# Kernel optimization log

Measured on AMD Instinct MI355X. Metric: run time of the kernel, lower is better.

## Reference

```python
import jax, jax.numpy as jnp
import numpy as np

ACT_MIN, ACT_MAX = -127.0, 127.0      # 8-bit symmetric
W_MIN, W_MAX = -127.0, 127.0          # 8-bit symmetric
B_MIN, B_MAX = -32767.0, 32767.0      # 16-bit symmetric
ALPHA = 10.0                          # clipped-ReLU ceiling


def fake_quant(x, min_v, max_v):
    # 'scale' quantization: per-tensor symmetric scale from max-abs,
    # round -> clamp -> dequant; straight-through estimator for grads.
    scale = max_v / jnp.max(jnp.abs(x))
    q = jnp.clip(jnp.round(x * scale), min_v, max_v) / scale
    return x + jax.lax.stop_gradient(q - x)


def qconv(x, w, b, stride, pad):
    wq = fake_quant(w, W_MIN, W_MAX)
    bq = fake_quant(b, B_MIN, B_MAX)
    y = jax.lax.conv_general_dilated(
        x, wq, (stride, stride), [(pad, pad), (pad, pad)],
        dimension_numbers=('NCHW', 'OIHW', 'NCHW'))
    return y + bq[None, :, None, None]


def qrelu(x):
    return fake_quant(jnp.clip(x, 0.0, ALPHA), ACT_MIN, ACT_MAX)


def maxpool(x, k, s, p):
    return jax.lax.reduce_window(
        x, -jnp.inf, jax.lax.max,
        (1, 1, k, k), (1, 1, s, s),
        [(0, 0), (0, 0), (p, p), (p, p)])


def setup_inputs() -> dict:
    key = jax.random.key(0)
    ks = jax.random.split(key, 13)

    def kaiming(k, shape):
        fan_in = int(np.prod(shape[1:]))
        return jax.random.normal(k, shape, jnp.float32) * np.sqrt(2.0 / fan_in)

    return {
        'x':  jax.random.normal(ks[0], (4096, 1, 32, 32), jnp.float32),
        'w1': kaiming(ks[1], (32, 1, 3, 3)),  'b1': jnp.zeros((32,), jnp.float32) + 0.01,
        'w2': kaiming(ks[2], (64, 32, 3, 3)), 'b2': jnp.zeros((64,), jnp.float32) + 0.01,
        'w3': kaiming(ks[3], (16, 64, 1, 1)), 'b3': jnp.zeros((16,), jnp.float32) + 0.01,
        'w4': kaiming(ks[4], (16, 16, 3, 3)), 'b4': jnp.zeros((16,), jnp.float32) + 0.01,
        'w5': kaiming(ks[5], (64, 16, 1, 1)), 'b5': jnp.zeros((64,), jnp.float32) + 0.01,
        'wl': kaiming(ks[6], (10, 64)),       'bl': jnp.zeros((10,), jnp.float32) + 0.01,
    }


def reference(x, w1, b1, w2, b2, w3, b3, w4, b4, w5, b5, wl, bl):
    x = fake_quant(x, ACT_MIN, ACT_MAX)           # quantize input acts
    x_skip1 = maxpool(x, 5, 4, 2)                 # [B,1,8,8]
    out = qrelu(qconv(x, w1, b1, 2, 1))           # [B,32,16,16]
    out = qconv(out, w2, b2, 2, 1)                # [B,64,8,8]
    out = qrelu(out + x_skip1)                    # broadcast 1ch skip over 64ch
    x_skip2 = maxpool(out, 3, 2, 1)               # [B,64,4,4]
    out = qrelu(qconv(out, w3, b3, 1, 0))         # [B,16,8,8]
    out = qrelu(qconv(out, w4, b4, 2, 1))         # [B,16,4,4]
    out = qconv(out, w5, b5, 1, 0)                # [B,64,4,4]
    out = qrelu(out + x_skip2)
    out = jnp.mean(out, axis=(2, 3))              # avgpool 4x4 -> [B,64]
    wq = fake_quant(wl, W_MIN, W_MAX)
    bq = fake_quant(bl, B_MIN, B_MAX)
    return out @ wq.T + bq                        # [B,10]
```

## Files before the change

kernel.cpp:

```cpp
#include <hip/hip_runtime.h>

#define BATCH 4096

typedef __attribute__((ext_vector_type(8))) short bf16x8;
typedef __attribute__((ext_vector_type(4))) float f32x4;

constexpr int OFF_MAXARR = 1024;
constexpr int OFF_W1Q = 8192;
constexpr int OFF_W2Q = OFF_W1Q + 288;
constexpr int OFF_W3Q = OFF_W2Q + 18432;
constexpr int OFF_W4Q = OFF_W3Q + 1024;
constexpr int OFF_W5Q = OFF_W4Q + 2304;
constexpr int OFF_WLQ = OFF_W5Q + 1024;
constexpr int OFF_B1Q = OFF_WLQ + 640;
constexpr int OFF_B2Q = OFF_B1Q + 32;
constexpr int OFF_B3Q = OFF_B2Q + 64;
constexpr int OFF_B4Q = OFF_B3Q + 16;
constexpr int OFF_B5Q = OFF_B4Q + 16;
constexpr int OFF_BLQ = OFF_B5Q + 64;
constexpr int OFF_W1I = 32768;
constexpr int OFF_W2I = OFF_W1I + 512;
constexpr int OFF_W3I = OFF_W2I + 9216;
constexpr size_t OFF_SK1F = 49152;
constexpr size_t OFF_V2   = OFF_SK1F + (size_t)BATCH * 64;
constexpr size_t OFF_SK2I = OFF_V2 + (size_t)BATCH * 4096;
constexpr size_t OFF_A3   = OFF_SK2I + (size_t)BATCH * 512;
constexpr size_t OFF_A4   = OFF_A3 + (size_t)BATCH * 1024;
constexpr size_t OFF_A5   = OFF_A4 + (size_t)BATCH * 256;
constexpr size_t WS_FLOATS_NEEDED = OFF_A5 + (size_t)BATCH * 1024;

#define A1_S   40
#define A1_ROW (18 * A1_S)

__device__ __forceinline__ float fq(float x, float scale, float maxv) {
    float q = rintf(x * scale);
    q = fminf(fmaxf(q, -maxv), maxv);
    return q / scale;
}

__device__ __forceinline__ short int_to_bf16_bits(float v) {
    return (short)(__float_as_uint(v) >> 16);
}

__device__ __forceinline__ float bf16_bits_to_float(short b) {
    return __uint_as_float(((unsigned)(unsigned short)b) << 16);
}

__device__ __forceinline__ void block_max_spread(float v, unsigned* arr, float* red4) {
#pragma unroll
    for (int off = 32; off; off >>= 1) v = fmaxf(v, __shfl_xor(v, off, 64));
    int tid = threadIdx.x;
    if ((tid & 63) == 0) red4[tid >> 6] = v;
    __syncthreads();
    if (tid == 0) {
        float m = fmaxf(fmaxf(red4[0], red4[1]), fmaxf(red4[2], red4[3]));
        atomicMax(&arr[(blockIdx.x & 63) << 4], __float_as_uint(m));
    }
    __syncthreads();
}

__device__ __forceinline__ float load_spread_max(const unsigned* arr, float* bc) {
    int tid = threadIdx.x;
    if (tid < 64) {
        float v = __uint_as_float(arr[tid << 4]);
#pragma unroll
        for (int off = 32; off; off >>= 1) v = fmaxf(v, __shfl_xor(v, off, 64));
        if (tid == 0) *bc = v;
    }
    __syncthreads();
    return *bc;
}

__device__ __forceinline__ void stage_xq(const float* xi, float sx, short* xt_q, int tid) {
    for (int i = tid; i < 1024; i += 256) {
        int ih = i >> 5, iw = i & 31;
        float q = rintf(xi[i] * sx);
        q = fminf(fmaxf(q, -127.f), 127.f);
        xt_q[(ih + 1) * 34 + (iw + 1)] = int_to_bf16_bits(q);
    }
}

__device__ __forceinline__ void build_qx1(const short* xt_q, short* qx1, int tid) {
    int oh = tid >> 4, ow = tid & 15;
    short* dst = qx1 + tid * 32;
#pragma unroll
    for (int kh = 0; kh < 3; kh++)
#pragma unroll
        for (int kw = 0; kw < 3; kw++)
            dst[kh * 3 + kw] = xt_q[(oh * 2 + kh) * 34 + (ow * 2 + kw)];
}

__device__ __forceinline__ void conv1_mfma(const short* qx1, const bf16x8 w1b[2],
                                           int lane, int wv, f32x4 acc[4][2]) {
#pragma unroll
    for (int mb = 0; mb < 4; mb++) {
        bf16x8 a = *(const bf16x8*)(qx1 + ((wv * 4 + mb) * 16 + (lane & 15)) * 32
                                    + (lane >> 4) * 8);
#pragma unroll
        for (int nb = 0; nb < 2; nb++)
            acc[mb][nb] = __builtin_amdgcn_mfma_f32_16x16x32_bf16(a, w1b[nb], acc[mb][nb], 0, 0, 0);
    }
}

struct WeightArgs {
    const float* src[12];
    float*       dst[12];
    int          n[12];
    float        maxv[12];
};

__global__ __launch_bounds__(256) void k_weights(WeightArgs a) {
    int t = blockIdx.x;
    const float* s = a.src[t];
    float* d = a.dst[t];
    int n = a.n[t];
    float maxv = a.maxv[t];
    __shared__ float red[256];
    int tid = threadIdx.x;
    float m = 0.f;
    for (int i = tid; i < n; i += 256) m = fmaxf(m, fabsf(s[i]));
    red[tid] = m;
    __syncthreads();
    for (int sft = 128; sft > 0; sft >>= 1) {
        if (tid < sft) red[tid] = fmaxf(red[tid], red[tid + sft]);
        __syncthreads();
    }
    float scale = maxv / red[0];
    for (int i = tid; i < n; i += 256) {
        float q = rintf(s[i] * scale);
        q = fminf(fmaxf(q, -maxv), maxv);
        d[i] = q / scale;
    }
}

__global__ __launch_bounds__(256) void k_prep_w1(const float* __restrict__ w1,
                                                 short* __restrict__ w1i,
                                                 float* __restrict__ inv_sw_slot) {
    __shared__ float red[256];
    int tid = threadIdx.x;
    float m = 0.f;
    for (int i = tid; i < 288; i += 256) m = fmaxf(m, fabsf(w1[i]));
    red[tid] = m;
    __syncthreads();
    for (int s = 128; s > 0; s >>= 1) {
        if (tid < s) red[tid] = fmaxf(red[tid], red[tid + s]);
        __syncthreads();
    }
    float maxw = red[0];
    float sw = 127.f / maxw;
    if (tid == 0) *inv_sw_slot = maxw / 127.f;
    for (int i = tid; i < 1024; i += 256) w1i[i] = 0;
    __syncthreads();
    for (int i = tid; i < 288; i += 256) {
        int oc = i / 9, t = i % 9;
        float q = rintf(w1[i] * sw);
        q = fminf(fmaxf(q, -127.f), 127.f);
        w1i[oc * 32 + t] = int_to_bf16_bits(q);
    }
}

__global__ __launch_bounds__(256) void k_prep_w2(const float* __restrict__ w2,
                                                 short* __restrict__ w2i,
                                                 float* __restrict__ inv_sw_slot) {
    __shared__ float red[256];
    int tid = threadIdx.x;
    float m = 0.f;
    for (int i = tid; i < 18432; i += 256) m = fmaxf(m, fabsf(w2[i]));
    red[tid] = m;
    __syncthreads();
    for (int s = 128; s > 0; s >>= 1) {
        if (tid < s) red[tid] = fmaxf(red[tid], red[tid + s]);
        __syncthreads();
    }
    float maxw = red[0];
    float sw = 127.f / maxw;
    if (tid == 0) *inv_sw_slot = maxw / 127.f;
    for (int i = tid; i < 18432; i += 256) {
        int oc = i / 288, r = i % 288, ic = r / 9, t = r % 9;
        float q = rintf(w2[i] * sw);
        q = fminf(fmaxf(q, -127.f), 127.f);
        w2i[oc * 288 + t * 32 + ic] = int_to_bf16_bits(q);
    }
}

__global__ __launch_bounds__(256) void k_prep_w3(const float* __restrict__ w3,
                                                 short* __restrict__ w3i,
                                                 float* __restrict__ inv_sw_slot) {
    __shared__ float red[256];
    int tid = threadIdx.x;
    float m = 0.f;
    for (int i = tid; i < 1024; i += 256) m = fmaxf(m, fabsf(w3[i]));
    red[tid] = m;
    __syncthreads();
    for (int s = 128; s > 0; s >>= 1) {
        if (tid < s) red[tid] = fmaxf(red[tid], red[tid + s]);
        __syncthreads();
    }
    float maxw = red[0];
    float sw = 127.f / maxw;
    if (tid == 0) *inv_sw_slot = maxw / 127.f;
    for (int i = tid; i < 1024; i += 256) {
        float q = rintf(w3[i] * sw);
        q = fminf(fmaxf(q, -127.f), 127.f);
        w3i[i] = int_to_bf16_bits(q);
    }
}

__global__ __launch_bounds__(256) void k_absmax(const float4* __restrict__ x, int n4,
                                                unsigned* arr) {
    __shared__ float red4[4];
    float m = 0.f;
    for (int i = blockIdx.x * 256 + threadIdx.x; i < n4; i += gridDim.x * 256) {
        float4 v = x[i];
        m = fmaxf(m, fmaxf(fmaxf(fabsf(v.x), fabsf(v.y)), fmaxf(fabsf(v.z), fabsf(v.w))));
    }
    block_max_spread(m, arr, red4);
}

__global__ __launch_bounds__(256) void k_s1(const float* __restrict__ x,
                                            const short* __restrict__ w1i,
                                            const float* __restrict__ b1q,
                                            const unsigned* xmaxarr,
                                            const float* __restrict__ inv_sw1p,
                                            float* __restrict__ skip1f,
                                            unsigned* m1arr) {
    __shared__ short xt_q[34 * 34];
    __shared__ short qx1[256 * 32];
    __shared__ float red4[4];
    __shared__ float bc0;
    int tid = threadIdx.x, lane = tid & 63, wv = tid >> 6;
    float xmax = load_spread_max(xmaxarr, &bc0);
    float sx = 127.f / xmax;
    float inv1 = (*inv_sw1p) / sx;
    bf16x8 w1b[2];
#pragma unroll
    for (int nb = 0; nb < 2; nb++)
        w1b[nb] = *(const bf16x8*)(w1i + (nb * 16 + (lane & 15)) * 32 + (lane >> 4) * 8);
    float bias1[2] = {b1q[lane & 15], b1q[16 + (lane & 15)]};

    for (int i = tid; i < 34 * 34; i += 256) xt_q[i] = 0;
    for (int i = tid; i < 256 * 16; i += 256) ((int*)qx1)[i] = 0;

    float lmax = 0.f;
    for (int li = 0; li < 4; li++) {
        int img = blockIdx.x * 4 + li;
        __syncthreads();
        stage_xq(x + (size_t)img * 1024, sx, xt_q, tid);
        __syncthreads();
        build_qx1(xt_q, qx1, tid);
        if (tid < 64) {
            int soh = tid >> 3, sow = tid & 7;
            float m = -INFINITY;
            int h0 = soh * 4 - 2, w0 = sow * 4 - 2;
            for (int kh = 0; kh < 5; kh++) {
                int ih = h0 + kh;
                if (ih < 0 || ih >= 32) continue;
                for (int kw = 0; kw < 5; kw++) {
                    int iw = w0 + kw;
                    if (iw < 0 || iw >= 32) continue;
                    m = fmaxf(m, bf16_bits_to_float(xt_q[(ih + 1) * 34 + (iw + 1)]));
                }
            }
            skip1f[img * 64 + tid] = m / sx;
        }
        __syncthreads();
        f32x4 acc[4][2] = {};
        conv1_mfma(qx1, w1b, lane, wv, acc);
#pragma unroll
        for (int mb = 0; mb < 4; mb++)
#pragma unroll
            for (int nb = 0; nb < 2; nb++)
#pragma unroll
                for (int r = 0; r < 4; r++) {
                    float v = acc[mb][nb][r] * inv1 + bias1[nb];
                    lmax = fmaxf(lmax, fminf(fmaxf(v, 0.f), 10.f));
                }
    }
    block_max_spread(lmax, m1arr, red4);
}

__global__ __launch_bounds__(256) void k_s2(const float* __restrict__ x,
                                            const short* __restrict__ w1i,
                                            const float* __restrict__ b1q,
                                            const short* __restrict__ w2i,
                                            const float* __restrict__ b2q,
                                            const float* __restrict__ skip1f,
                                            const unsigned* xmaxarr, const unsigned* m1arr,
                                            const float* __restrict__ inv_sw1p,
                                            const float* __restrict__ inv_sw2p,
                                            float* __restrict__ v2w,
                                            unsigned* m2arr) {
    __shared__ short xt_q[34 * 34];
    __shared__ short qx1[256 * 32];
    __shared__ short a1t[18 * A1_ROW];
    __shared__ float sk1s[64];
    __shared__ float red4[4];
    __shared__ float bc0, bc1;
    int tid = threadIdx.x, lane = tid & 63, wv = tid >> 6;
    float xmax = load_spread_max(xmaxarr, &bc0);
    float m1 = load_spread_max(m1arr, &bc1);
    float sx = 127.f / xmax;
    float inv1 = (*inv_sw1p) / sx;
    float s1q = 127.f / m1;
    float inv2 = (m1 / 127.f) * (*inv_sw2p);

    bf16x8 w1b[2];
#pragma unroll
    for (int nb = 0; nb < 2; nb++)
        w1b[nb] = *(const bf16x8*)(w1i + (nb * 16 + (lane & 15)) * 32 + (lane >> 4) * 8);
    float bias1[2] = {b1q[lane & 15], b1q[16 + (lane & 15)]};
    int oc2 = wv * 16 + (lane & 15);
    bf16x8 bw2[9];
#pragma unroll
    for (int t = 0; t < 9; t++)
        bw2[t] = *(const bf16x8*)(w2i + oc2 * 288 + t * 32 + (lane >> 4) * 8);
    float bias2 = b2q[oc2];

    for (int i = tid; i < 34 * 34; i += 256) xt_q[i] = 0;
    for (int i = tid; i < 256 * 16; i += 256) ((int*)qx1)[i] = 0;
    for (int i = tid; i < 18 * A1_ROW / 2; i += 256) ((int*)a1t)[i] = 0;

    float lmax = 0.f;
    for (int li = 0; li < 4; li++) {
        int img = blockIdx.x * 4 + li;
        __syncthreads();
        stage_xq(x + (size_t)img * 1024, sx, xt_q, tid);
        if (tid < 64) sk1s[tid] = skip1f[img * 64 + tid];
        __syncthreads();
        build_qx1(xt_q, qx1, tid);
        __syncthreads();
        f32x4 acc1[4][2] = {};
        conv1_mfma(qx1, w1b, lane, wv, acc1);
#pragma unroll
        for (int mb = 0; mb < 4; mb++)
#pragma unroll
            for (int nb = 0; nb < 2; nb++)
#pragma unroll
                for (int r = 0; r < 4; r++) {
                    float v = acc1[mb][nb][r] * inv1 + bias1[nb];
                    v = fminf(fmaxf(v, 0.f), 10.f);
                    float q = fminf(rintf(v * s1q), 127.f);
                    int pos = (wv * 4 + mb) * 16 + (lane >> 4) * 4 + r;
                    int oc = nb * 16 + (lane & 15);
                    a1t[((pos >> 4) + 1) * A1_ROW + ((pos & 15) + 1) * A1_S + oc] =
                        int_to_bf16_bits(q);
                }
        __syncthreads();
        float* vo = v2w + (size_t)img * 4096;
#pragma unroll
        for (int mb = 0; mb < 4; mb++) {
            int m = mb * 16 + (lane & 15);
            int oh = m >> 3, ow = m & 7;
            const short* abase = a1t + (oh * 2) * A1_ROW + (ow * 2) * A1_S + (lane >> 4) * 8;
            f32x4 acc = {0.f, 0.f, 0.f, 0.f};
#pragma unroll
            for (int kh = 0; kh < 3; kh++)
#pragma unroll
                for (int kw = 0; kw < 3; kw++) {
                    bf16x8 av = *(const bf16x8*)(abase + kh * A1_ROW + kw * A1_S);
                    acc = __builtin_amdgcn_mfma_f32_16x16x32_bf16(av, bw2[kh * 3 + kw], acc, 0, 0, 0);
                }
            float4 vv;
            float* vvp = (float*)&vv;
#pragma unroll
            for (int r = 0; r < 4; r++) {
                int pos = mb * 16 + (lane >> 4) * 4 + r;
                float v = acc[r] * inv2 + bias2 + sk1s[pos];
                v = fminf(fmaxf(v, 0.f), 10.f);
                vvp[r] = v;
                lmax = fmaxf(lmax, v);
            }
            *(float4*)(vo + oc2 * 64 + mb * 16 + (lane >> 4) * 4) = vv;
        }
    }
    block_max_spread(lmax, m2arr, red4);
}

__global__ __launch_bounds__(256) void k_s3(const float* __restrict__ v2w,
                                            const short* __restrict__ w3i,
                                            const float* __restrict__ b3q,
                                            const unsigned* m2arr,
                                            const float* __restrict__ inv_sw3p,
                                            float* __restrict__ a3w,
                                            short* __restrict__ sk2q,
                                            unsigned* m3arr) {
    __shared__ short a2q[64 * 64];
    __shared__ float red4[4];
    __shared__ float bc0;
    int tid = threadIdx.x, lane = tid & 63, wv = tid >> 6;
    float m2 = load_spread_max(m2arr, &bc0);
    float s2 = 127.f / m2;
    float inv3 = (m2 / 127.f) * (*inv_sw3p);
    int oc2 = wv * 16 + (lane & 15);
    bf16x8 bw3[2];
#pragma unroll
    for (int t = 0; t < 2; t++)
        bw3[t] = *(const bf16x8*)(w3i + (lane & 15) * 64 + t * 32 + (lane >> 4) * 8);
    float bias3 = b3q[lane & 15];

    float lmax = 0.f;
    for (int li = 0; li < 4; li++) {
        int img = blockIdx.x * 4 + li;
        __syncthreads();
        const float* vi = v2w + (size_t)img * 4096;
#pragma unroll
        for (int mb = 0; mb < 4; mb++) {
            float4 vv = *(const float4*)(vi + oc2 * 64 + mb * 16 + (lane >> 4) * 4);
            const float* vvp = (const float*)&vv;
#pragma unroll
            for (int r = 0; r < 4; r++) {
                int pos = mb * 16 + (lane >> 4) * 4 + r;
                float q = fminf(rintf(vvp[r] * s2), 127.f);
                a2q[pos * 64 + oc2] = int_to_bf16_bits(q);
            }
        }
        __syncthreads();
        const short* abase = a2q + (wv * 16 + (lane & 15)) * 64 + (lane >> 4) * 8;
        f32x4 acc = {0.f, 0.f, 0.f, 0.f};
#pragma unroll
        for (int t = 0; t < 2; t++) {
            bf16x8 av = *(const bf16x8*)(abase + t * 32);
            acc = __builtin_amdgcn_mfma_f32_16x16x32_bf16(av, bw3[t], acc, 0, 0, 0);
        }
        float* a3o = a3w + (size_t)img * 1024;
#pragma unroll
        for (int r = 0; r < 4; r++) {
            int pos = wv * 16 + (lane >> 4) * 4 + r;
            float v = acc[r] * inv3 + bias3;
            v = fminf(fmaxf(v, 0.f), 10.f);
            a3o[(lane & 15) * 64 + pos] = v;
            lmax = fmaxf(lmax, v);
        }
        short* sko = sk2q + (size_t)img * 1024;
#pragma unroll
        for (int r = 0; r < 4; ++r) {
            int idx = tid * 4 + r;
            int c = idx >> 4, pp = idx & 15, soh = pp >> 2, sow = pp & 3;
            float m = -INFINITY;
            for (int kh = 0; kh < 3; kh++) {
                int ih = soh * 2 - 1 + kh;
                if (ih < 0 || ih >= 8) continue;
                for (int kw = 0; kw < 3; kw++) {
                    int iw = sow * 2 - 1 + kw;
                    if (iw < 0 || iw >= 8) continue;
                    m = fmaxf(m, bf16_bits_to_float(a2q[(ih * 8 + iw) * 64 + c]));
                }
            }
            sko[idx] = int_to_bf16_bits(m);
        }
    }
    block_max_spread(lmax, m3arr, red4);
}

__global__ __launch_bounds__(256) void k_conv4(const float* __restrict__ a3,
                                               const float* __restrict__ w4q,
                                               const float* __restrict__ b4q,
                                               const unsigned* m3arr,
                                               float* __restrict__ a4,
                                               unsigned* m4arr) {
    __shared__ float tile[16 * 10 * 10];
    __shared__ float red4[4];
    __shared__ float bc0;
    int b = blockIdx.x, tid = threadIdx.x;
    float m3 = load_spread_max(m3arr, &bc0);
    float s3 = 127.f / m3;
    for (int i = tid; i < 1600; i += 256) tile[i] = 0.f;
    __syncthreads();
    const float* ai = a3 + (size_t)b * 1024;
    for (int i = tid; i < 1024; i += 256) {
        int ic = i >> 6, p = i & 63, ih = p >> 3, iw = p & 7;
        float q = rintf(ai[i] * s3);
        q = fminf(fmaxf(q, -127.f), 127.f);
        tile[ic * 100 + (ih + 1) * 10 + (iw + 1)] = q / s3;
    }
    __syncthreads();
    int oc = tid >> 4, p = tid & 15, oh = p >> 2, ow = p & 3;
    float acc = b4q[oc];
    const float* w = w4q + oc * 144;
    for (int ic = 0; ic < 16; ic++) {
        const float* tin = tile + ic * 100 + (oh * 2) * 10 + (ow * 2);
        const float* wc = w + ic * 9;
#pragma unroll
        for (int kh = 0; kh < 3; kh++)
#pragma unroll
            for (int kw = 0; kw < 3; kw++)
                acc += tin[kh * 10 + kw] * wc[kh * 3 + kw];
    }
    float v = fminf(fmaxf(acc, 0.f), 10.f);
    a4[(size_t)b * 256 + tid] = v;
    block_max_spread(v, m4arr, red4);
}

__global__ __launch_bounds__(256) void k_conv5(const float* __restrict__ a4,
                                               const float* __restrict__ w5q,
                                               const float* __restrict__ b5q,
                                               const short* __restrict__ sk2q,
                                               const unsigned* m2arr,
                                               const unsigned* m4arr,
                                               float* __restrict__ a5,
                                               unsigned* m5arr) {
    __shared__ float tin[256];
    __shared__ float red4[4];
    __shared__ float bc0, bc1;
    int b = blockIdx.x, tid = threadIdx.x;
    float m2 = load_spread_max(m2arr, &bc0);
    float m4 = load_spread_max(m4arr, &bc1);
    float s4 = 127.f / m4;
    float invs2 = m2 / 127.f;
    const float* ai = a4 + (size_t)b * 256;
    {
        float q = rintf(ai[tid] * s4);
        q = fminf(fmaxf(q, -127.f), 127.f);
        tin[tid] = q / s4;
    }
    __syncthreads();
    int p = tid & 15, ocb = tid >> 4;
    float lmax = 0.f;
    float* o = a5 + (size_t)b * 1024;
    for (int j = 0; j < 4; j++) {
        int oc = ocb * 4 + j;
        float acc = b5q[oc];
        const float* w = w5q + oc * 16;
#pragma unroll
        for (int ic = 0; ic < 16; ic++) acc += tin[ic * 16 + p] * w[ic];
        acc += bf16_bits_to_float(sk2q[(size_t)b * 1024 + oc * 16 + p]) * invs2;
        float v = fminf(fmaxf(acc, 0.f), 10.f);
        o[oc * 16 + p] = v;
        lmax = fmaxf(lmax, v);
    }
    block_max_spread(lmax, m5arr, red4);
}

__global__ __launch_bounds__(64) void k_head(const float* __restrict__ a5,
                                             const unsigned* m5arr,
                                             const float* __restrict__ wlq,
                                             const float* __restrict__ blq,
                                             float* __restrict__ out) {
    __shared__ float h[64];
    __shared__ float bc0;
    int b = blockIdx.x, c = threadIdx.x;
    float m5 = load_spread_max(m5arr, &bc0);
    float s5 = 127.f / m5;
    const float* ai = a5 + (size_t)b * 1024 + c * 16;
    float sum = 0.f;
#pragma unroll
    for (int p = 0; p < 16; p++) sum += fq(ai[p], s5, 127.f);
    h[c] = sum * (1.f / 16.f);
    __syncthreads();
    if (c < 10) {
        float acc = blq[c];
        const float* w = wlq + c * 64;
        for (int ic = 0; ic < 64; ic++) acc = fmaf(h[ic], w[ic], acc);
        out[(size_t)b * 10 + c] = acc;
    }
}

extern "C" void kernel_launch(void* const* d_in, const int* in_sizes, int n_in,
                              void* d_out, int out_size, void* d_ws, size_t ws_size,
                              hipStream_t stream) {
    const float* x  = (const float*)d_in[0];
    const float* w1 = (const float*)d_in[1];
    const float* b1 = (const float*)d_in[2];
    const float* w2 = (const float*)d_in[3];
    const float* b2 = (const float*)d_in[4];
    const float* w3 = (const float*)d_in[5];
    const float* b3 = (const float*)d_in[6];
    const float* w4 = (const float*)d_in[7];
    const float* b4 = (const float*)d_in[8];
    const float* w5 = (const float*)d_in[9];
    const float* b5 = (const float*)d_in[10];
    const float* wl = (const float*)d_in[11];
    const float* bl = (const float*)d_in[12];

    if (ws_size < WS_FLOATS_NEEDED * sizeof(float)) return;

    float* ws = (float*)d_ws;
    unsigned* slots = (unsigned*)d_ws;
    unsigned* marr[6];
    for (int k = 0; k < 6; k++) marr[k] = slots + OFF_MAXARR + k * 1024;
    short* w1i = (short*)(ws + OFF_W1I);
    short* w2i = (short*)(ws + OFF_W2I);
    short* w3i = (short*)(ws + OFF_W3I);

    hipMemsetAsync(d_ws, 0, 32768, stream);

    WeightArgs wa;
    const float* srcs[12] = {w1, w2, w3, w4, w5, wl, b1, b2, b3, b4, b5, bl};
    const int    ns[12]   = {288, 18432, 1024, 2304, 1024, 640, 32, 64, 16, 16, 64, 10};
    const int    offs[12] = {OFF_W1Q, OFF_W2Q, OFF_W3Q, OFF_W4Q, OFF_W5Q, OFF_WLQ,
                             OFF_B1Q, OFF_B2Q, OFF_B3Q, OFF_B4Q, OFF_B5Q, OFF_BLQ};
    const float  mv[12]   = {127.f, 127.f, 127.f, 127.f, 127.f, 127.f,
                             32767.f, 32767.f, 32767.f, 32767.f, 32767.f, 32767.f};
    for (int i = 0; i < 12; i++) {
        wa.src[i] = srcs[i];
        wa.dst[i] = ws + offs[i];
        wa.n[i] = ns[i];
        wa.maxv[i] = mv[i];
    }
    k_weights<<<12, 256, 0, stream>>>(wa);
    k_prep_w1<<<1, 256, 0, stream>>>(w1, w1i, ws + 8);
    k_prep_w2<<<1, 256, 0, stream>>>(w2, w2i, ws + 6);
    k_prep_w3<<<1, 256, 0, stream>>>(w3, w3i, ws + 7);

    k_absmax<<<512, 256, 0, stream>>>((const float4*)x, BATCH * 256, marr[0]);
    k_s1<<<BATCH / 4, 256, 0, stream>>>(x, w1i, ws + OFF_B1Q, marr[0], ws + 8,
                                        ws + OFF_SK1F, marr[1]);
    k_s2<<<BATCH / 4, 256, 0, stream>>>(x, w1i, ws + OFF_B1Q, w2i, ws + OFF_B2Q,
                                        ws + OFF_SK1F, marr[0], marr[1], ws + 8, ws + 6,
                                        ws + OFF_V2, marr[2]);
    k_s3<<<BATCH / 4, 256, 0, stream>>>(ws + OFF_V2, w3i, ws + OFF_B3Q, marr[2], ws + 7,
                                        ws + OFF_A3, (short*)(ws + OFF_SK2I), marr[3]);
    k_conv4<<<BATCH, 256, 0, stream>>>(ws + OFF_A3, ws + OFF_W4Q, ws + OFF_B4Q, marr[3],
                                       ws + OFF_A4, marr[4]);
    k_conv5<<<BATCH, 256, 0, stream>>>(ws + OFF_A4, ws + OFF_W5Q, ws + OFF_B5Q,
                                       (const short*)(ws + OFF_SK2I), marr[2], marr[4],
                                       ws + OFF_A5, marr[5]);
    k_head<<<BATCH, 64, 0, stream>>>(ws + OFF_A5, marr[5], ws + OFF_WLQ, ws + OFF_BLQ,
                                     (float*)d_out);
}
```

Before: 255.7 us.

## Merge prep kernels into one launch and build conv1 fragments directly from LDS

Folds the five weight/bias/input absmax prep kernels into a single launch that dispatches work by block index, with 256 blocks (previously 512) for the input absmax. It also drops the qx1 im2col staging buffer in k_s1/k_s2, gathering conv1 MFMA A-fragments straight from the padded input tile. This removes launch overhead, one LDS round trip and a barrier per image, and frees 16KB of LDS per block. The cost is scattered 2-byte LDS reads when forming each fragment and less parallelism in the absmax pass.

```diff
diff --git a/kernel.cpp b/kernel.cpp
--- a/kernel.cpp
+++ b/kernel.cpp
@@ -80,141 +80,118 @@
     }
 }
 
-__device__ __forceinline__ void build_qx1(const short* xt_q, short* qx1, int tid) {
-    int oh = tid >> 4, ow = tid & 15;
-    short* dst = qx1 + tid * 32;
-#pragma unroll
-    for (int kh = 0; kh < 3; kh++)
-#pragma unroll
-        for (int kw = 0; kw < 3; kw++)
-            dst[kh * 3 + kw] = xt_q[(oh * 2 + kh) * 34 + (ow * 2 + kw)];
-}
-
-__device__ __forceinline__ void conv1_mfma(const short* qx1, const bf16x8 w1b[2],
-                                           int lane, int wv, f32x4 acc[4][2]) {
-#pragma unroll
-    for (int mb = 0; mb < 4; mb++) {
-        bf16x8 a = *(const bf16x8*)(qx1 + ((wv * 4 + mb) * 16 + (lane & 15)) * 32
-                                    + (lane >> 4) * 8);
-#pragma unroll
-        for (int nb = 0; nb < 2; nb++)
-            acc[mb][nb] = __builtin_amdgcn_mfma_f32_16x16x32_bf16(a, w1b[nb], acc[mb][nb], 0, 0, 0);
-    }
-}
-
-struct WeightArgs {
+__device__ __forceinline__ bf16x8 load_a1frag(const short* xt_q, int pos, int kslot) {
+    bf16x8 a = {0, 0, 0, 0, 0, 0, 0, 0};
+    int oh = pos >> 4, ow = pos & 15;
+    const short* base = xt_q + (oh * 2) * 34 + ow * 2;
+    if (kslot == 0) {
+        a[0] = base[0];  a[1] = base[1];  a[2] = base[2];
+        a[3] = base[34]; a[4] = base[35]; a[5] = base[36];
+        a[6] = base[68]; a[7] = base[69];
+    } else if (kslot == 1) {
+        a[0] = base[70];
+    }
+    return a;
+}
+
+struct PrepArgs {
     const float* src[12];
     float*       dst[12];
     int          n[12];
     float        maxv[12];
+    const float* w1; short* w1i; float* inv1;
+    const float* w2; short* w2i; float* inv2;
+    const float* w3; short* w3i; float* inv3;
+    const float4* x; int n4; unsigned* xarr;
 };
 
-__global__ __launch_bounds__(256) void k_weights(WeightArgs a) {
-    int t = blockIdx.x;
-    const float* s = a.src[t];
-    float* d = a.dst[t];
-    int n = a.n[t];
-    float maxv = a.maxv[t];
+__global__ __launch_bounds__(256) void k_prep(PrepArgs P) {
     __shared__ float red[256];
-    int tid = threadIdx.x;
-    float m = 0.f;
-    for (int i = tid; i < n; i += 256) m = fmaxf(m, fabsf(s[i]));
-    red[tid] = m;
-    __syncthreads();
-    for (int sft = 128; sft > 0; sft >>= 1) {
-        if (tid < sft) red[tid] = fmaxf(red[tid], red[tid + sft]);
-        __syncthreads();
-    }
-    float scale = maxv / red[0];
-    for (int i = tid; i < n; i += 256) {
-        float q = rintf(s[i] * scale);
-        q = fminf(fmaxf(q, -maxv), maxv);
-        d[i] = q / scale;
-    }
-}
-
-__global__ __launch_bounds__(256) void k_prep_w1(const float* __restrict__ w1,
-                                                 short* __restrict__ w1i,
-                                                 float* __restrict__ inv_sw_slot) {
-    __shared__ float red[256];
-    int tid = threadIdx.x;
-    float m = 0.f;
-    for (int i = tid; i < 288; i += 256) m = fmaxf(m, fabsf(w1[i]));
-    red[tid] = m;
-    __syncthreads();
-    for (int s = 128; s > 0; s >>= 1) {
-        if (tid < s) red[tid] = fmaxf(red[tid], red[tid + s]);
-        __syncthreads();
-    }
-    float maxw = red[0];
-    float sw = 127.f / maxw;
-    if (tid == 0) *inv_sw_slot = maxw / 127.f;
-    for (int i = tid; i < 1024; i += 256) w1i[i] = 0;
-    __syncthreads();
-    for (int i = tid; i < 288; i += 256) {
-        int oc = i / 9, t = i % 9;
-        float q = rintf(w1[i] * sw);
-        q = fminf(fmaxf(q, -127.f), 127.f);
-        w1i[oc * 32 + t] = int_to_bf16_bits(q);
-    }
-}
-
-__global__ __launch_bounds__(256) void k_prep_w2(const float* __restrict__ w2,
-                                                 short* __restrict__ w2i,
-                                                 float* __restrict__ inv_sw_slot) {
-    __shared__ float red[256];
-    int tid = threadIdx.x;
-    float m = 0.f;
-    for (int i = tid; i < 18432; i += 256) m = fmaxf(m, fabsf(w2[i]));
-    red[tid] = m;
-    __syncthreads();
-    for (int s = 128; s > 0; s >>= 1) {
-        if (tid < s) red[tid] = fmaxf(red[tid], red[tid + s]);
-        __syncthreads();
-    }
-    float maxw = red[0];
-    float sw = 127.f / maxw;
-    if (tid == 0) *inv_sw_slot = maxw / 127.f;
-    for (int i = tid; i < 18432; i += 256) {
-        int oc = i / 288, r = i % 288, ic = r / 9, t = r % 9;
-        float q = rintf(w2[i] * sw);
-        q = fminf(fmaxf(q, -127.f), 127.f);
-        w2i[oc * 288 + t * 32 + ic] = int_to_bf16_bits(q);
-    }
-}
-
-__global__ __launch_bounds__(256) void k_prep_w3(const float* __restrict__ w3,
-                                                 short* __restrict__ w3i,
-                                                 float* __restrict__ inv_sw_slot) {
-    __shared__ float red[256];
-    int tid = threadIdx.x;
-    float m = 0.f;
-    for (int i = tid; i < 1024; i += 256) m = fmaxf(m, fabsf(w3[i]));
-    red[tid] = m;
-    __syncthreads();
-    for (int s = 128; s > 0; s >>= 1) {
-        if (tid < s) red[tid] = fmaxf(red[tid], red[tid + s]);
-        __syncthreads();
-    }
-    float maxw = red[0];
-    float sw = 127.f / maxw;
-    if (tid == 0) *inv_sw_slot = maxw / 127.f;
-    for (int i = tid; i < 1024; i += 256) {
-        float q = rintf(w3[i] * sw);
-        q = fminf(fmaxf(q, -127.f), 127.f);
-        w3i[i] = int_to_bf16_bits(q);
-    }
-}
-
-__global__ __launch_bounds__(256) void k_absmax(const float4* __restrict__ x, int n4,
-                                                unsigned* arr) {
     __shared__ float red4[4];
-    float m = 0.f;
-    for (int i = blockIdx.x * 256 + threadIdx.x; i < n4; i += gridDim.x * 256) {
-        float4 v = x[i];
-        m = fmaxf(m, fmaxf(fmaxf(fabsf(v.x), fabsf(v.y)), fmaxf(fabsf(v.z), fabsf(v.w))));
-    }
-    block_max_spread(m, arr, red4);
+    int b = blockIdx.x, tid = threadIdx.x;
+    if (b < 12) {
+        const float* s = P.src[b];
+        float* d = P.dst[b];
+        int n = P.n[b];
+        float maxv = P.maxv[b];
+        float m = 0.f;
+        for (int i = tid; i < n; i += 256) m = fmaxf(m, fabsf(s[i]));
+        red[tid] = m;
+        __syncthreads();
+        for (int sft = 128; sft > 0; sft >>= 1) {
+            if (tid < sft) red[tid] = fmaxf(red[tid], red[tid + sft]);
+            __syncthreads();
+        }
+        float scale = maxv / red[0];
+        for (int i = tid; i < n; i += 256) {
+            float q = rintf(s[i] * scale);
+            q = fminf(fmaxf(q, -maxv), maxv);
+            d[i] = q / scale;
+        }
+    } else if (b == 12) {
+        float m = 0.f;
+        for (int i = tid; i < 288; i += 256) m = fmaxf(m, fabsf(P.w1[i]));
+        red[tid] = m;
+        __syncthreads();
+        for (int s = 128; s > 0; s >>= 1) {
+            if (tid < s) red[tid] = fmaxf(red[tid], red[tid + s]);
+            __syncthreads();
+        }
+        float maxw = red[0];
+        float sw = 127.f / maxw;
+        if (tid == 0) *P.inv1 = maxw / 127.f;
+        for (int i = tid; i < 1024; i += 256) P.w1i[i] = 0;
+        __syncthreads();
+        for (int i = tid; i < 288; i += 256) {
+            int oc = i / 9, t = i % 9;
+            float q = rintf(P.w1[i] * sw);
+            q = fminf(fmaxf(q, -127.f), 127.f);
+            P.w1i[oc * 32 + t] = int_to_bf16_bits(q);
+        }
+    } else if (b == 13) {
+        float m = 0.f;
+        for (int i = tid; i < 18432; i += 256) m = fmaxf(m, fabsf(P.w2[i]));
+        red[tid] = m;
+        __syncthreads();
+        for (int s = 128; s > 0; s >>= 1) {
+            if (tid < s) red[tid] = fmaxf(red[tid], red[tid + s]);
+            __syncthreads();
+        }
+        float maxw = red[0];
+        float sw = 127.f / maxw;
+        if (tid == 0) *P.inv2 = maxw / 127.f;
+        for (int i = tid; i < 18432; i += 256) {
+            int oc = i / 288, r = i % 288, ic = r / 9, t = r % 9;
+            float q = rintf(P.w2[i] * sw);
+            q = fminf(fmaxf(q, -127.f), 127.f);
+            P.w2i[oc * 288 + t * 32 + ic] = int_to_bf16_bits(q);
+        }
+    } else if (b == 14) {
+        float m = 0.f;
+        for (int i = tid; i < 1024; i += 256) m = fmaxf(m, fabsf(P.w3[i]));
+        red[tid] = m;
+        __syncthreads();
+        for (int s = 128; s > 0; s >>= 1) {
+            if (tid < s) red[tid] = fmaxf(red[tid], red[tid + s]);
+            __syncthreads();
+        }
+        float maxw = red[0];
+        float sw = 127.f / maxw;
+        if (tid == 0) *P.inv3 = maxw / 127.f;
+        for (int i = tid; i < 1024; i += 256) {
+            float q = rintf(P.w3[i] * sw);
+            q = fminf(fmaxf(q, -127.f), 127.f);
+            P.w3i[i] = int_to_bf16_bits(q);
+        }
+    } else {
+        float m = 0.f;
+        int nb = gridDim.x - 15;
+        for (int i = (b - 15) * 256 + tid; i < P.n4; i += nb * 256) {
+            float4 v = P.x[i];
+            m = fmaxf(m, fmaxf(fmaxf(fabsf(v.x), fabsf(v.y)), fmaxf(fabsf(v.z), fabsf(v.w))));
+        }
+        block_max_spread(m, P.xarr, red4);
+    }
 }
 
 __global__ __launch_bounds__(256) void k_s1(const float* __restrict__ x,
@@ -225,21 +202,20 @@
                                             float* __restrict__ skip1f,
                                             unsigned* m1arr) {
     __shared__ short xt_q[34 * 34];
-    __shared__ short qx1[256 * 32];
     __shared__ float red4[4];
     __shared__ float bc0;
     int tid = threadIdx.x, lane = tid & 63, wv = tid >> 6;
+    int kslot = lane >> 4;
     float xmax = load_spread_max(xmaxarr, &bc0);
     float sx = 127.f / xmax;
     float inv1 = (*inv_sw1p) / sx;
     bf16x8 w1b[2];
 #pragma unroll
     for (int nb = 0; nb < 2; nb++)
-        w1b[nb] = *(const bf16x8*)(w1i + (nb * 16 + (lane & 15)) * 32 + (lane >> 4) * 8);
+        w1b[nb] = *(const bf16x8*)(w1i + (nb * 16 + (lane & 15)) * 32 + kslot * 8);
     float bias1[2] = {b1q[lane & 15], b1q[16 + (lane & 15)]};
 
     for (int i = tid; i < 34 * 34; i += 256) xt_q[i] = 0;
-    for (int i = tid; i < 256 * 16; i += 256) ((int*)qx1)[i] = 0;
 
     float lmax = 0.f;
     for (int li = 0; li < 4; li++) {
@@ -247,7 +223,6 @@
         __syncthreads();
         stage_xq(x + (size_t)img * 1024, sx, xt_q, tid);
         __syncthreads();
-        build_qx1(xt_q, qx1, tid);
         if (tid < 64) {
             int soh = tid >> 3, sow = tid & 7;
             float m = -INFINITY;
@@ -263,9 +238,14 @@
             }
             skip1f[img * 64 + tid] = m / sx;
         }
-        __syncthreads();
         f32x4 acc[4][2] = {};
-        conv1_mfma(qx1, w1b, lane, wv, acc);
+#pragma unroll
+        for (int mb = 0; mb < 4; mb++) {
+            bf16x8 a = load_a1frag(xt_q, (wv * 4 + mb) * 16 + (lane & 15), kslot);
+#pragma unroll
+            for (int nb = 0; nb < 2; nb++)
+                acc[mb][nb] = __builtin_amdgcn_mfma_f32_16x16x32_bf16(a, w1b[nb], acc[mb][nb], 0, 0, 0);
+        }
 #pragma unroll
         for (int mb = 0; mb < 4; mb++)
 #pragma unroll
@@ -291,12 +271,12 @@
                                             float* __restrict__ v2w,
                                             unsigned* m2arr) {
     __shared__ short xt_q[34 * 34];
-    __shared__ short qx1[256 * 32];
     __shared__ short a1t[18 * A1_ROW];
     __shared__ float sk1s[64];
     __shared__ float red4[4];
     __shared__ float bc0, bc1;
     int tid = threadIdx.x, lane = tid & 63, wv = tid >> 6;
+    int kslot = lane >> 4;
     float xmax = load_spread_max(xmaxarr, &bc0);
     float m1 = load_spread_max(m1arr, &bc1);
     float sx = 127.f / xmax;
@@ -307,17 +287,16 @@
     bf16x8 w1b[2];
 #pragma unroll
     for (int nb = 0; nb < 2; nb++)
-        w1b[nb] = *(const bf16x8*)(w1i + (nb * 16 + (lane & 15)) * 32 + (lane >> 4) * 8);
+        w1b[nb] = *(const bf16x8*)(w1i + (nb * 16 + (lane & 15)) * 32 + kslot * 8);
     float bias1[2] = {b1q[lane & 15], b1q[16 + (lane & 15)]};
     int oc2 = wv * 16 + (lane & 15);
     bf16x8 bw2[9];
 #pragma unroll
     for (int t = 0; t < 9; t++)
-        bw2[t] = *(const bf16x8*)(w2i + oc2 * 288 + t * 32 + (lane >> 4) * 8);
+        bw2[t] = *(const bf16x8*)(w2i + oc2 * 288 + t * 32 + kslot * 8);
     float bias2 = b2q[oc2];
 
     for (int i = tid; i < 34 * 34; i += 256) xt_q[i] = 0;
-    for (int i = tid; i < 256 * 16; i += 256) ((int*)qx1)[i] = 0;
     for (int i = tid; i < 18 * A1_ROW / 2; i += 256) ((int*)a1t)[i] = 0;
 
     float lmax = 0.f;
@@ -327,10 +306,14 @@
         stage_xq(x + (size_t)img * 1024, sx, xt_q, tid);
         if (tid < 64) sk1s[tid] = skip1f[img * 64 + tid];
         __syncthreads();
-        build_qx1(xt_q, qx1, tid);
-        __syncthreads();
         f32x4 acc1[4][2] = {};
-        conv1_mfma(qx1, w1b, lane, wv, acc1);
+#pragma unroll
+        for (int mb = 0; mb < 4; mb++) {
+            bf16x8 a = load_a1frag(xt_q, (wv * 4 + mb) * 16 + (lane & 15), kslot);
+#pragma unroll
+            for (int nb = 0; nb < 2; nb++)
+                acc1[mb][nb] = __builtin_amdgcn_mfma_f32_16x16x32_bf16(a, w1b[nb], acc1[mb][nb], 0, 0, 0);
+        }
 #pragma unroll
         for (int mb = 0; mb < 4; mb++)
 #pragma unroll
@@ -351,7 +334,7 @@
         for (int mb = 0; mb < 4; mb++) {
             int m = mb * 16 + (lane & 15);
             int oh = m >> 3, ow = m & 7;
-            const short* abase = a1t + (oh * 2) * A1_ROW + (ow * 2) * A1_S + (lane >> 4) * 8;
+            const short* abase = a1t + (oh * 2) * A1_ROW + (ow * 2) * A1_S + kslot * 8;
             f32x4 acc = {0.f, 0.f, 0.f, 0.f};
 #pragma unroll
             for (int kh = 0; kh < 3; kh++)
@@ -584,7 +567,7 @@
 
     hipMemsetAsync(d_ws, 0, 32768, stream);
 
-    WeightArgs wa;
+    PrepArgs P;
     const float* srcs[12] = {w1, w2, w3, w4, w5, wl, b1, b2, b3, b4, b5, bl};
     const int    ns[12]   = {288, 18432, 1024, 2304, 1024, 640, 32, 64, 16, 16, 64, 10};
     const int    offs[12] = {OFF_W1Q, OFF_W2Q, OFF_W3Q, OFF_W4Q, OFF_W5Q, OFF_WLQ,
@@ -592,17 +575,17 @@
     const float  mv[12]   = {127.f, 127.f, 127.f, 127.f, 127.f, 127.f,
                              32767.f, 32767.f, 32767.f, 32767.f, 32767.f, 32767.f};
     for (int i = 0; i < 12; i++) {
-        wa.src[i] = srcs[i];
-        wa.dst[i] = ws + offs[i];
-        wa.n[i] = ns[i];
-        wa.maxv[i] = mv[i];
-    }
-    k_weights<<<12, 256, 0, stream>>>(wa);
-    k_prep_w1<<<1, 256, 0, stream>>>(w1, w1i, ws + 8);
-    k_prep_w2<<<1, 256, 0, stream>>>(w2, w2i, ws + 6);
-    k_prep_w3<<<1, 256, 0, stream>>>(w3, w3i, ws + 7);
-
-    k_absmax<<<512, 256, 0, stream>>>((const float4*)x, BATCH * 256, marr[0]);
+        P.src[i] = srcs[i];
+        P.dst[i] = ws + offs[i];
+        P.n[i] = ns[i];
+        P.maxv[i] = mv[i];
+    }
+    P.w1 = w1; P.w1i = w1i; P.inv1 = ws + 8;
+    P.w2 = w2; P.w2i = w2i; P.inv2 = ws + 6;
+    P.w3 = w3; P.w3i = w3i; P.inv3 = ws + 7;
+    P.x = (const float4*)x; P.n4 = BATCH * 256; P.xarr = marr[0];
+
+    k_prep<<<15 + 256, 256, 0, stream>>>(P);
     k_s1<<<BATCH / 4, 256, 0, stream>>>(x, w1i, ws + OFF_B1Q, marr[0], ws + 8,
                                         ws + OFF_SK1F, marr[1]);
     k_s2<<<BATCH / 4, 256, 0, stream>>>(x, w1i, ws + OFF_B1Q, w2i, ws + OFF_B2Q,
```

After: 210.6 us. -17.6%, faster.
